# Optimization experiments

Measured on AMD Instinct MI355X. Metric: run time of the kernel, lower is better.

## Reference

```python
import jax, jax.numpy as jnp
import numpy as np

TOL = 1e-4
MAX_ITER = 50
D = 512
B = 16384

def setup_inputs() -> dict:
    key = jax.random.key(0)
    kx, kw = jax.random.split(key)
    x = jax.random.normal(kx, (B, D), dtype=jnp.float32)
    # nn.Linear default init: U(-1/sqrt(d), 1/sqrt(d)), bias=False
    bound = 1.0 / np.sqrt(D)
    W = jax.random.uniform(kw, (D, D), dtype=jnp.float32, minval=-bound, maxval=bound)
    return {"x": x, "W": W}

def reference(x, W):
    # Fixed-point iteration z <- tanh(z @ W^T + x).
    # Torch uses a data-dependent while loop with early break; here we run a
    # fixed-length scan and freeze z once the convergence criterion fires,
    # which reproduces the same converged value (z is held constant after
    # ||z_next - z|| < tol, exactly like breaking out of the loop).
    z0 = jnp.zeros_like(x)

    def step(carry, _):
        z, done = carry
        z_next = jnp.tanh(z @ W.T + x)          # [B, D]
        err = jnp.linalg.norm(z_next - z)        # global Frobenius norm, like torch.norm
        z_new = jnp.where(done, z, z_next)       # freeze after convergence (early-exit)
        done = done | (err < TOL)
        return (z_new, done), None

    (z, _), _ = jax.lax.scan(step, (z0, jnp.array(False)), None, length=MAX_ITER)
    return z
```

## Files before the change

kernel.cpp:

```cpp
#include <hip/hip_runtime.h>


typedef short s8v  __attribute__((ext_vector_type(8)));
typedef float f32x16 __attribute__((ext_vector_type(16)));
typedef _Float16 h4 __attribute__((ext_vector_type(4)));

#define BATCH 16384
#define DIM   512
#define TM    32
#define NITER 50

#define KSC 2.8853900817779268f

__device__ __forceinline__ unsigned short f2bf(float f) {
    unsigned int u = __float_as_uint(f);
    u += 0x7fffu + ((u >> 16) & 1u);
    return (unsigned short)(u >> 16);
}

__global__ void wprep_kernel(const float* __restrict__ W, unsigned short* __restrict__ Wf) {
    int tid = blockIdx.x * blockDim.x + threadIdx.x;
    int jt  = tid >> 11;
    int rem = tid & 2047;
    int ks  = rem >> 6;
    int L   = rem & 63;
    int j   = jt * 32 + (L & 31);
    int k   = ks * 16 + (L >> 5) * 8;
    const float* src = W + j * DIM + k;
    uint4 p;
    p.x = (unsigned)f2bf(src[0] * KSC) | ((unsigned)f2bf(src[1] * KSC) << 16);
    p.y = (unsigned)f2bf(src[2] * KSC) | ((unsigned)f2bf(src[3] * KSC) << 16);
    p.z = (unsigned)f2bf(src[4] * KSC) | ((unsigned)f2bf(src[5] * KSC) << 16);
    p.w = (unsigned)f2bf(src[6] * KSC) | ((unsigned)f2bf(src[7] * KSC) << 16);
    ((uint4*)Wf)[tid] = p;
}

__device__ __forceinline__ int z_addr(int r, int j) {
    int c  = j >> 3;
    int lo = j & 7;
    return r * DIM + (((c ^ (r & 7)) << 3) | lo);
}

__device__ __forceinline__ unsigned pk_bf16(float lo, float hi) {
    unsigned r;
    asm("v_cvt_pk_bf16_f32 %0, %1, %2" : "=v"(r) : "v"(lo), "v"(hi));
    return r;
}

__device__ __forceinline__ float tanh_pre(float s) {
    float t = __builtin_amdgcn_exp2f(s);
    float q = __builtin_amdgcn_rcpf(t + 1.0f);
    return fmaf(-2.0f, q, 1.0f);
}

__device__ __forceinline__ f32x16 zero16() {
    f32x16 v;
#pragma unroll
    for (int i = 0; i < 16; ++i) v[i] = 0.0f;
    return v;
}

__device__ __forceinline__ h4 cvt_h4(float4 t) {
    h4 r;
    r[0] = (_Float16)t.x; r[1] = (_Float16)t.y;
    r[2] = (_Float16)t.z; r[3] = (_Float16)t.w;
    return r;
}

__global__ __launch_bounds__(512, 2)
void fixpoint_kernel(const float* __restrict__ x,
                     const unsigned short* __restrict__ Wf,
                     float* __restrict__ out) {
    __shared__ alignas(16) unsigned short zt[2][TM * DIM];

    const int tid  = threadIdx.x;
    const int lane = tid & 63;
    const int w    = tid >> 6;
    const int l31  = lane & 31;
    const int h    = lane >> 5;
    const int r0   = blockIdx.x * TM;
    const int jt0  = 2 * w;
    const int jb0  = 64 * w;
    const int swz  = l31 & 7;

    const s8v* Wfv = (const s8v*)Wf;

    h4 xa[4], xb[4];
    {
        const float* xr0 = x + (size_t)(r0 + l31) * DIM;
#pragma unroll
        for (int g = 0; g < 4; ++g) {
            const int j0 = jb0 + 8 * g + 4 * h;
            xa[g] = cvt_h4(*(const float4*)&xr0[j0]);
            xb[g] = cvt_h4(*(const float4*)&xr0[j0 + 32]);
        }
    }

    f32x16 ac0, ac1;

    auto epi_z = [&](unsigned short* __restrict__ zn) {
#pragma unroll
        for (int g = 0; g < 4; ++g) {
            const int j0 = jb0 + 8 * g + 4 * h;
            uint2 p;
            p.x = pk_bf16(tanh_pre(fmaf((float)xa[g][0], KSC, ac0[4*g+0])),
                          tanh_pre(fmaf((float)xa[g][1], KSC, ac0[4*g+1])));
            p.y = pk_bf16(tanh_pre(fmaf((float)xa[g][2], KSC, ac0[4*g+2])),
                          tanh_pre(fmaf((float)xa[g][3], KSC, ac0[4*g+3])));
            *(uint2*)&zn[z_addr(l31, j0)] = p;
            p.x = pk_bf16(tanh_pre(fmaf((float)xb[g][0], KSC, ac1[4*g+0])),
                          tanh_pre(fmaf((float)xb[g][1], KSC, ac1[4*g+1])));
            p.y = pk_bf16(tanh_pre(fmaf((float)xb[g][2], KSC, ac1[4*g+2])),
                          tanh_pre(fmaf((float)xb[g][3], KSC, ac1[4*g+3])));
            *(uint2*)&zn[z_addr(l31, j0 + 32)] = p;
        }
    };

    auto epi_out = [&]() {
        float* o0 = out + (size_t)(r0 + l31) * DIM;
#pragma unroll
        for (int g = 0; g < 4; ++g) {
            const int j0 = jb0 + 8 * g + 4 * h;
            float4 v;
            v.x = tanh_pre(fmaf((float)xa[g][0], KSC, ac0[4*g+0]));
            v.y = tanh_pre(fmaf((float)xa[g][1], KSC, ac0[4*g+1]));
            v.z = tanh_pre(fmaf((float)xa[g][2], KSC, ac0[4*g+2]));
            v.w = tanh_pre(fmaf((float)xa[g][3], KSC, ac0[4*g+3]));
            *(float4*)&o0[j0] = v;
            v.x = tanh_pre(fmaf((float)xb[g][0], KSC, ac1[4*g+0]));
            v.y = tanh_pre(fmaf((float)xb[g][1], KSC, ac1[4*g+1]));
            v.z = tanh_pre(fmaf((float)xb[g][2], KSC, ac1[4*g+2]));
            v.w = tanh_pre(fmaf((float)xb[g][3], KSC, ac1[4*g+3]));
            *(float4*)&o0[j0 + 32] = v;
        }
    };

    auto gemm = [&](const unsigned short* __restrict__ zc) {
        ac0 = zero16(); ac1 = zero16();
#pragma unroll 4
        for (int ks = 0; ks < 32; ++ks) {
            s8v a0 = Wfv[(jt0 * 32 + ks) * 64 + lane];
            s8v a1 = Wfv[((jt0 + 1) * 32 + ks) * 64 + lane];
            const int c = ((2 * ks + h) ^ swz) << 3;
            s8v b0 = *(const s8v*)&zc[l31 * DIM + c];
            ac0 = __builtin_amdgcn_mfma_f32_32x32x16_bf16(a0, b0, ac0, 0, 0, 0);
            ac1 = __builtin_amdgcn_mfma_f32_32x32x16_bf16(a1, b0, ac1, 0, 0, 0);
        }
    };

    ac0 = zero16(); ac1 = zero16();
    epi_z(zt[0]);
    __syncthreads();

    int cur = 0;
#pragma unroll 1
    for (int it = 0; it < NITER - 2; ++it) {
        gemm(zt[cur]);
        epi_z(zt[cur ^ 1]);
        __syncthreads();
        cur ^= 1;
    }
    gemm(zt[cur]);
    epi_out();
}

extern "C" void kernel_launch(void* const* d_in, const int* in_sizes, int n_in,
                              void* d_out, int out_size, void* d_ws, size_t ws_size,
                              hipStream_t stream) {
    const float* x = (const float*)d_in[0];
    const float* W = (const float*)d_in[1];
    float* out = (float*)d_out;
    unsigned short* Wf = (unsigned short*)d_ws;

    wprep_kernel<<<128, 256, 0, stream>>>(W, Wf);
    fixpoint_kernel<<<BATCH / TM, 512, 0, stream>>>(x, Wf, out);
}
```

Baseline: 583.6 us.

## Double row tile to 64 and weave the first-half tanh epilogue into the second GEMM

Each block now handles 64 batch rows instead of 32. Each loaded W fragment feeds two MFMAs over two row halves, which halves W reads per row. The GEMM is split into two column-tile passes, and the tanh/bf16 store for the first tile's accumulators is interleaved into the second tile's MFMA loop so VALU work can overlap matrix work. The cost is a 128KB double-buffered LDS tile per block, which likely allows only one block per CU and halves resident waves. It also needs more registers for four accumulators and four x fragment sets.

```diff
diff --git a/kernel.cpp b/kernel.cpp
--- a/kernel.cpp
+++ b/kernel.cpp
@@ -7,7 +7,7 @@
 
 #define BATCH 16384
 #define DIM   512
-#define TM    32
+#define TM    64
 #define NITER 50
 
 #define KSC 2.8853900817779268f
@@ -85,82 +85,123 @@
 
     const s8v* Wfv = (const s8v*)Wf;
 
-    h4 xa[4], xb[4];
+    h4 xf0[4], xf1[4], xf2[4], xf3[4];
     {
         const float* xr0 = x + (size_t)(r0 + l31) * DIM;
+        const float* xr1 = x + (size_t)(r0 + l31 + 32) * DIM;
 #pragma unroll
         for (int g = 0; g < 4; ++g) {
             const int j0 = jb0 + 8 * g + 4 * h;
-            xa[g] = cvt_h4(*(const float4*)&xr0[j0]);
-            xb[g] = cvt_h4(*(const float4*)&xr0[j0 + 32]);
+            xf0[g] = cvt_h4(*(const float4*)&xr0[j0]);
+            xf1[g] = cvt_h4(*(const float4*)&xr1[j0]);
+            xf2[g] = cvt_h4(*(const float4*)&xr0[j0 + 32]);
+            xf3[g] = cvt_h4(*(const float4*)&xr1[j0 + 32]);
         }
     }
 
-    f32x16 ac0, ac1;
-
-    auto epi_z = [&](unsigned short* __restrict__ zn) {
-#pragma unroll
-        for (int g = 0; g < 4; ++g) {
-            const int j0 = jb0 + 8 * g + 4 * h;
-            uint2 p;
-            p.x = pk_bf16(tanh_pre(fmaf((float)xa[g][0], KSC, ac0[4*g+0])),
-                          tanh_pre(fmaf((float)xa[g][1], KSC, ac0[4*g+1])));
-            p.y = pk_bf16(tanh_pre(fmaf((float)xa[g][2], KSC, ac0[4*g+2])),
-                          tanh_pre(fmaf((float)xa[g][3], KSC, ac0[4*g+3])));
-            *(uint2*)&zn[z_addr(l31, j0)] = p;
-            p.x = pk_bf16(tanh_pre(fmaf((float)xb[g][0], KSC, ac1[4*g+0])),
-                          tanh_pre(fmaf((float)xb[g][1], KSC, ac1[4*g+1])));
-            p.y = pk_bf16(tanh_pre(fmaf((float)xb[g][2], KSC, ac1[4*g+2])),
-                          tanh_pre(fmaf((float)xb[g][3], KSC, ac1[4*g+3])));
-            *(uint2*)&zn[z_addr(l31, j0 + 32)] = p;
+    f32x16 p0, p1, q0, q1;
+
+    auto epi_q = [&](unsigned short* __restrict__ zn, int tb, int g,
+                     const f32x16& A, int row, h4 xg) {
+        const int j0 = jb0 + tb + 8 * g + 4 * h;
+        uint2 pv;
+        pv.x = pk_bf16(tanh_pre(fmaf((float)xg[0], KSC, A[4*g+0])),
+                       tanh_pre(fmaf((float)xg[1], KSC, A[4*g+1])));
+        pv.y = pk_bf16(tanh_pre(fmaf((float)xg[2], KSC, A[4*g+2])),
+                       tanh_pre(fmaf((float)xg[3], KSC, A[4*g+3])));
+        *(uint2*)&zn[z_addr(row, j0)] = pv;
+    };
+
+    auto gemm0 = [&](const unsigned short* __restrict__ zc) {
+        p0 = zero16(); p1 = zero16();
+#pragma unroll 4
+        for (int ks = 0; ks < 32; ++ks) {
+            s8v a = Wfv[(jt0 * 32 + ks) * 64 + lane];
+            const int c = ((2 * ks + h) ^ swz) << 3;
+            s8v b0 = *(const s8v*)&zc[l31 * DIM + c];
+            s8v b1 = *(const s8v*)&zc[(l31 + 32) * DIM + c];
+            p0 = __builtin_amdgcn_mfma_f32_32x32x16_bf16(a, b0, p0, 0, 0, 0);
+            p1 = __builtin_amdgcn_mfma_f32_32x32x16_bf16(a, b1, p1, 0, 0, 0);
+        }
+    };
+
+    auto gemm1_weave = [&](const unsigned short* __restrict__ zc,
+                           unsigned short* __restrict__ zn) {
+        q0 = zero16(); q1 = zero16();
+#pragma unroll
+        for (int ch = 0; ch < 8; ++ch) {
+#pragma unroll
+            for (int k2 = 0; k2 < 4; ++k2) {
+                const int ks = ch * 4 + k2;
+                s8v a = Wfv[((jt0 + 1) * 32 + ks) * 64 + lane];
+                const int c = ((2 * ks + h) ^ swz) << 3;
+                s8v b0 = *(const s8v*)&zc[l31 * DIM + c];
+                s8v b1 = *(const s8v*)&zc[(l31 + 32) * DIM + c];
+                q0 = __builtin_amdgcn_mfma_f32_32x32x16_bf16(a, b0, q0, 0, 0, 0);
+                q1 = __builtin_amdgcn_mfma_f32_32x32x16_bf16(a, b1, q1, 0, 0, 0);
+            }
+            const int g = ch >> 1;
+            if ((ch & 1) == 0) epi_q(zn, 0, g, p0, l31,      xf0[g]);
+            else               epi_q(zn, 0, g, p1, l31 + 32, xf1[g]);
         }
     };
 
     auto epi_out = [&]() {
         float* o0 = out + (size_t)(r0 + l31) * DIM;
+        float* o1 = out + (size_t)(r0 + l31 + 32) * DIM;
 #pragma unroll
         for (int g = 0; g < 4; ++g) {
             const int j0 = jb0 + 8 * g + 4 * h;
             float4 v;
-            v.x = tanh_pre(fmaf((float)xa[g][0], KSC, ac0[4*g+0]));
-            v.y = tanh_pre(fmaf((float)xa[g][1], KSC, ac0[4*g+1]));
-            v.z = tanh_pre(fmaf((float)xa[g][2], KSC, ac0[4*g+2]));
-            v.w = tanh_pre(fmaf((float)xa[g][3], KSC, ac0[4*g+3]));
+            v.x = tanh_pre(fmaf((float)xf0[g][0], KSC, p0[4*g+0]));
+            v.y = tanh_pre(fmaf((float)xf0[g][1], KSC, p0[4*g+1]));
+            v.z = tanh_pre(fmaf((float)xf0[g][2], KSC, p0[4*g+2]));
+            v.w = tanh_pre(fmaf((float)xf0[g][3], KSC, p0[4*g+3]));
             *(float4*)&o0[j0] = v;
-            v.x = tanh_pre(fmaf((float)xb[g][0], KSC, ac1[4*g+0]));
-            v.y = tanh_pre(fmaf((float)xb[g][1], KSC, ac1[4*g+1]));
-            v.z = tanh_pre(fmaf((float)xb[g][2], KSC, ac1[4*g+2]));
-            v.w = tanh_pre(fmaf((float)xb[g][3], KSC, ac1[4*g+3]));
+            v.x = tanh_pre(fmaf((float)xf1[g][0], KSC, p1[4*g+0]));
+            v.y = tanh_pre(fmaf((float)xf1[g][1], KSC, p1[4*g+1]));
+            v.z = tanh_pre(fmaf((float)xf1[g][2], KSC, p1[4*g+2]));
+            v.w = tanh_pre(fmaf((float)xf1[g][3], KSC, p1[4*g+3]));
+            *(float4*)&o1[j0] = v;
+            v.x = tanh_pre(fmaf((float)xf2[g][0], KSC, q0[4*g+0]));
+            v.y = tanh_pre(fmaf((float)xf2[g][1], KSC, q0[4*g+1]));
+            v.z = tanh_pre(fmaf((float)xf2[g][2], KSC, q0[4*g+2]));
+            v.w = tanh_pre(fmaf((float)xf2[g][3], KSC, q0[4*g+3]));
             *(float4*)&o0[j0 + 32] = v;
-        }
-    };
-
-    auto gemm = [&](const unsigned short* __restrict__ zc) {
-        ac0 = zero16(); ac1 = zero16();
-#pragma unroll 4
-        for (int ks = 0; ks < 32; ++ks) {
-            s8v a0 = Wfv[(jt0 * 32 + ks) * 64 + lane];
-            s8v a1 = Wfv[((jt0 + 1) * 32 + ks) * 64 + lane];
-            const int c = ((2 * ks + h) ^ swz) << 3;
-            s8v b0 = *(const s8v*)&zc[l31 * DIM + c];
-            ac0 = __builtin_amdgcn_mfma_f32_32x32x16_bf16(a0, b0, ac0, 0, 0, 0);
-            ac1 = __builtin_amdgcn_mfma_f32_32x32x16_bf16(a1, b0, ac1, 0, 0, 0);
-        }
-    };
-
-    ac0 = zero16(); ac1 = zero16();
-    epi_z(zt[0]);
+            v.x = tanh_pre(fmaf((float)xf3[g][0], KSC, q1[4*g+0]));
+            v.y = tanh_pre(fmaf((float)xf3[g][1], KSC, q1[4*g+1]));
+            v.z = tanh_pre(fmaf((float)xf3[g][2], KSC, q1[4*g+2]));
+            v.w = tanh_pre(fmaf((float)xf3[g][3], KSC, q1[4*g+3]));
+            *(float4*)&o1[j0 + 32] = v;
+        }
+    };
+
+    p0 = zero16(); p1 = zero16();
+#pragma unroll
+    for (int g = 0; g < 4; ++g) {
+        epi_q(zt[0], 0,  g, p0, l31,      xf0[g]);
+        epi_q(zt[0], 0,  g, p1, l31 + 32, xf1[g]);
+        epi_q(zt[0], 32, g, p0, l31,      xf2[g]);
+        epi_q(zt[0], 32, g, p1, l31 + 32, xf3[g]);
+    }
     __syncthreads();
 
     int cur = 0;
 #pragma unroll 1
     for (int it = 0; it < NITER - 2; ++it) {
-        gemm(zt[cur]);
-        epi_z(zt[cur ^ 1]);
+        unsigned short* zn = zt[cur ^ 1];
+        gemm0(zt[cur]);
+        gemm1_weave(zt[cur], zn);
+#pragma unroll
+        for (int g = 0; g < 4; ++g) {
+            epi_q(zn, 32, g, q0, l31,      xf2[g]);
+            epi_q(zn, 32, g, q1, l31 + 32, xf3[g]);
+        }
         __syncthreads();
         cur ^= 1;
     }
-    gemm(zt[cur]);
+    gemm0(zt[cur]);
+    gemm1_weave(zt[cur], zt[cur ^ 1]);
     epi_out();
 }
 
```

New measurement: 600.0 us. 1.03x slower.

## Double row tile to 64 and reuse each W fragment across two row tiles

Applied to the files above, without the earlier changes.

Each block now processes 64 batch rows with 16 waves, each wave owning a 32-column output tile and computing it for two 32-row halves. One W fragment load now feeds two MFMAs instead of one per unique W tile, halving global/L2 traffic for W, and the first two k-slices of W are kept in registers across iterations. This doubles LDS per block to the full z double buffer for 64 rows, reducing blocks per CU and increasing barrier cost per iteration; the launch bounds hint may also constrain registers.

```diff
diff --git a/kernel.cpp b/kernel.cpp
--- a/kernel.cpp
+++ b/kernel.cpp
@@ -7,7 +7,7 @@
 
 #define BATCH 16384
 #define DIM   512
-#define TM    32
+#define TM    64
 #define NITER 50
 
 #define KSC 2.8853900817779268f
@@ -67,7 +67,7 @@
     return r;
 }
 
-__global__ __launch_bounds__(512, 2)
+__global__ __launch_bounds__(1024, 4)
 void fixpoint_kernel(const float* __restrict__ x,
                      const unsigned short* __restrict__ Wf,
                      float* __restrict__ out) {
@@ -79,8 +79,7 @@
     const int l31  = lane & 31;
     const int h    = lane >> 5;
     const int r0   = blockIdx.x * TM;
-    const int jt0  = 2 * w;
-    const int jb0  = 64 * w;
+    const int jb0  = 32 * w;
     const int swz  = l31 & 7;
 
     const s8v* Wfv = (const s8v*)Wf;
@@ -88,13 +87,17 @@
     h4 xa[4], xb[4];
     {
         const float* xr0 = x + (size_t)(r0 + l31) * DIM;
+        const float* xr1 = x + (size_t)(r0 + l31 + 32) * DIM;
 #pragma unroll
         for (int g = 0; g < 4; ++g) {
             const int j0 = jb0 + 8 * g + 4 * h;
             xa[g] = cvt_h4(*(const float4*)&xr0[j0]);
-            xb[g] = cvt_h4(*(const float4*)&xr0[j0 + 32]);
+            xb[g] = cvt_h4(*(const float4*)&xr1[j0]);
         }
     }
+
+    const s8v a_h0 = Wfv[(w * 32 + 0) * 64 + lane];
+    const s8v a_h1 = Wfv[(w * 32 + 1) * 64 + lane];
 
     f32x16 ac0, ac1;
 
@@ -112,12 +115,13 @@
                           tanh_pre(fmaf((float)xb[g][1], KSC, ac1[4*g+1])));
             p.y = pk_bf16(tanh_pre(fmaf((float)xb[g][2], KSC, ac1[4*g+2])),
                           tanh_pre(fmaf((float)xb[g][3], KSC, ac1[4*g+3])));
-            *(uint2*)&zn[z_addr(l31, j0 + 32)] = p;
+            *(uint2*)&zn[z_addr(l31 + 32, j0)] = p;
         }
     };
 
     auto epi_out = [&]() {
         float* o0 = out + (size_t)(r0 + l31) * DIM;
+        float* o1 = out + (size_t)(r0 + l31 + 32) * DIM;
 #pragma unroll
         for (int g = 0; g < 4; ++g) {
             const int j0 = jb0 + 8 * g + 4 * h;
@@ -131,20 +135,32 @@
             v.y = tanh_pre(fmaf((float)xb[g][1], KSC, ac1[4*g+1]));
             v.z = tanh_pre(fmaf((float)xb[g][2], KSC, ac1[4*g+2]));
             v.w = tanh_pre(fmaf((float)xb[g][3], KSC, ac1[4*g+3]));
-            *(float4*)&o0[j0 + 32] = v;
+            *(float4*)&o1[j0] = v;
         }
     };
 
     auto gemm = [&](const unsigned short* __restrict__ zc) {
         ac0 = zero16(); ac1 = zero16();
-#pragma unroll 4
-        for (int ks = 0; ks < 32; ++ks) {
-            s8v a0 = Wfv[(jt0 * 32 + ks) * 64 + lane];
-            s8v a1 = Wfv[((jt0 + 1) * 32 + ks) * 64 + lane];
+        {
+            int c = (h ^ swz) << 3;
+            s8v b0 = *(const s8v*)&zc[l31 * DIM + c];
+            s8v b1 = *(const s8v*)&zc[(l31 + 32) * DIM + c];
+            ac0 = __builtin_amdgcn_mfma_f32_32x32x16_bf16(a_h0, b0, ac0, 0, 0, 0);
+            ac1 = __builtin_amdgcn_mfma_f32_32x32x16_bf16(a_h0, b1, ac1, 0, 0, 0);
+            c = ((2 + h) ^ swz) << 3;
+            b0 = *(const s8v*)&zc[l31 * DIM + c];
+            b1 = *(const s8v*)&zc[(l31 + 32) * DIM + c];
+            ac0 = __builtin_amdgcn_mfma_f32_32x32x16_bf16(a_h1, b0, ac0, 0, 0, 0);
+            ac1 = __builtin_amdgcn_mfma_f32_32x32x16_bf16(a_h1, b1, ac1, 0, 0, 0);
+        }
+#pragma unroll 6
+        for (int ks = 2; ks < 32; ++ks) {
+            s8v a = Wfv[(w * 32 + ks) * 64 + lane];
             const int c = ((2 * ks + h) ^ swz) << 3;
             s8v b0 = *(const s8v*)&zc[l31 * DIM + c];
-            ac0 = __builtin_amdgcn_mfma_f32_32x32x16_bf16(a0, b0, ac0, 0, 0, 0);
-            ac1 = __builtin_amdgcn_mfma_f32_32x32x16_bf16(a1, b0, ac1, 0, 0, 0);
+            s8v b1 = *(const s8v*)&zc[(l31 + 32) * DIM + c];
+            ac0 = __builtin_amdgcn_mfma_f32_32x32x16_bf16(a, b0, ac0, 0, 0, 0);
+            ac1 = __builtin_amdgcn_mfma_f32_32x32x16_bf16(a, b1, ac1, 0, 0, 0);
         }
     };
 
@@ -173,5 +189,5 @@
     unsigned short* Wf = (unsigned short*)d_ws;
 
     wprep_kernel<<<128, 256, 0, stream>>>(W, Wf);
-    fixpoint_kernel<<<BATCH / TM, 512, 0, stream>>>(x, Wf, out);
+    fixpoint_kernel<<<BATCH / TM, 1024, 0, stream>>>(x, Wf, out);
 }
```

Result: faster. 506.6 us (-13.2%).
